# Optimization experiments

Hardware: AMD Instinct MI355X
Metric: run time of the kernel (lower is better)

The kernel has to match this reference:

```python
import jax, jax.numpy as jnp
import numpy as np

BS, SEQ, FT_IN = 64, 576, 768
HID, HEADS, FT_OUT = 512, 4, 512
N = SEQ + 1  # pooled node + tokens
NUM_NODES = BS * N


def _build_edges():
    # star graph per sample: 0 <-> (1+j) both directions, then self loops, batched with offsets
    j = np.arange(SEQ)
    src = np.empty(2 * SEQ, np.int32); dst = np.empty(2 * SEQ, np.int32)
    src[0::2] = 0;      dst[0::2] = 1 + j
    src[1::2] = 1 + j;  dst[1::2] = 0
    loops = np.arange(N, dtype=np.int32)
    src = np.concatenate([src, loops]); dst = np.concatenate([dst, loops])
    offs = (np.arange(BS, dtype=np.int32) * N)[:, None]
    return (src[None, :] + offs).reshape(-1), (dst[None, :] + offs).reshape(-1)


def setup_inputs() -> dict:
    key = jax.random.key(0)
    ks = jax.random.split(key, 24)
    s = 0.02
    src, dst = _build_edges()
    return {
        "hidden_states": jax.random.normal(ks[0], (BS, SEQ, FT_IN), jnp.float32),
        "pooled_output": jax.random.normal(ks[1], (BS, HID), jnp.float32),
        # SeqLinear projector: 768 -> 512 -> 512
        "pw1": jax.random.normal(ks[2], (FT_IN, HID)) * s, "pb1": jnp.zeros((HID,)),
        "pw2": jax.random.normal(ks[3], (HID, HID)) * s, "pb2": jnp.zeros((HID,)),
        # GATv2 conv1: 512 -> 4 heads x 128
        "wl1": jax.random.normal(ks[4], (HID, HID)) * s, "bl1": jnp.zeros((HID,)),
        "wr1": jax.random.normal(ks[5], (HID, HID)) * s, "br1": jnp.zeros((HID,)),
        "att1": jax.random.normal(ks[6], (HEADS, HID // HEADS)) * s,
        "bias1": jnp.zeros((HID,)),
        # GATv2 conv2: 512 -> 1 head x 512
        "wl2": jax.random.normal(ks[7], (HID, HID)) * s, "bl2": jnp.zeros((HID,)),
        "wr2": jax.random.normal(ks[8], (HID, HID)) * s, "br2": jnp.zeros((HID,)),
        "att2": jax.random.normal(ks[9], (1, HID)) * s,
        "bias2": jnp.zeros((HID,)),
        # final lin: 512 -> 512
        "linw": jax.random.normal(ks[10], (HID, FT_OUT)) * s, "linb": jnp.zeros((FT_OUT,)),
        "src": jnp.asarray(src), "dst": jnp.asarray(dst),
    }


def _gatv2(x, src, dst, wl, bl, wr, br, att, bias, heads, cout, num_nodes):
    # PyG GATv2Conv (share_weights=False), eval mode (attn dropout off)
    xl = (x @ wl + bl).reshape(num_nodes, heads, cout)  # source transform (messages)
    xr = (x @ wr + br).reshape(num_nodes, heads, cout)  # target transform
    z = jax.nn.leaky_relu(xl[src] + xr[dst], negative_slope=0.2)  # [E,H,C]
    e = jnp.einsum('ehc,hc->eh', z, att)                          # [E,H]
    m = jax.ops.segment_max(e, dst, num_segments=num_nodes)
    p = jnp.exp(e - m[dst])
    s = jax.ops.segment_sum(p, dst, num_segments=num_nodes)
    alpha = p / (s[dst] + 1e-16)                                  # segment softmax over in-edges
    out = jax.ops.segment_sum(xl[src] * alpha[..., None], dst, num_segments=num_nodes)
    return out.reshape(num_nodes, heads * cout) + bias


def reference(hidden_states, pooled_output, pw1, pb1, pw2, pb2,
              wl1, bl1, wr1, br1, att1, bias1,
              wl2, bl2, wr2, br2, att2, bias2,
              linw, linb, src, dst):
    bs, seq, _ = hidden_states.shape
    n = seq + 1
    num_nodes = bs * n
    # ProjLayers / SeqLinear (eval: dropout identity); GELU between layers
    h = jax.nn.gelu(hidden_states @ pw1 + pb1)
    h = h @ pw2 + pb2                                    # [bs, seq, 512]
    x = jnp.concatenate([pooled_output[:, None, :], h], axis=1)  # [bs, n, 512]
    x = x.reshape(num_nodes, -1)
    # GNN: GATv2 -> GELU -> GATv2
    h1 = jax.nn.gelu(_gatv2(x, src, dst, wl1, bl1, wr1, br1, att1, bias1, HEADS, HID // HEADS, num_nodes))
    h2 = _gatv2(h1, src, dst, wl2, bl2, wr2, br2, att2, bias2, 1, HID, num_nodes)
    h2b = h2.reshape(bs, n, -1)
    graph_mean = h2b.mean(axis=1)                        # global_mean_pool (contiguous graphs)
    cls = h2b[:, 0, :]                                   # node 0 per graph; dropout off (eval)
    out = cls @ linw + linb + pooled_output
    return out, graph_mean
```

## Files before the change

kernel.cpp:

```cpp
#include <hip/hip_runtime.h>
#include <hip/hip_bf16.h>
#include <math.h>

constexpr int BSZ       = 64;
constexpr int SEQL      = 576;
constexpr int FTIN      = 768;
constexpr int HID       = 512;
constexpr int NNODE     = SEQL + 1;
constexpr int NUM_NODES = BSZ * NNODE;
constexpr int MROWS     = BSZ * SEQL;

using b8 = __attribute__((ext_vector_type(8))) __bf16;
using f4 = __attribute__((ext_vector_type(4))) float;
typedef unsigned short u16;

__device__ __forceinline__ float gelu_f(float x) {
    float x3 = x * x * x;
    return 0.5f * x * (1.0f + tanhf(0.7978845608028654f * (x + 0.044715f * x3)));
}
__device__ __forceinline__ float lrelu(float x) {
    return x > 0.0f ? x : 0.2f * x;
}
__device__ __forceinline__ u16 f2bf(float v) {
    __hip_bfloat16 b = __float2bfloat16(v);
    return __builtin_bit_cast(u16, b);
}
__device__ __forceinline__ float bf2f(u16 u) {
    return __bfloat162float(__builtin_bit_cast(__hip_bfloat16, u));
}
__device__ __forceinline__ void split_bf(float v, u16& h, u16& l) {
    h = f2bf(v);
    l = f2bf(v - bf2f(h));
}
__device__ __forceinline__ void gl16(const void* g, void* l) {
    __builtin_amdgcn_global_load_lds(
        (const __attribute__((address_space(1))) unsigned int*)g,
        (__attribute__((address_space(3))) unsigned int*)l, 16, 0, 0);
}
__device__ __forceinline__ f4 mfma16(b8 a, b8 b, f4 c) {
    return __builtin_amdgcn_mfma_f32_16x16x32_bf16(a, b, c, 0, 0, 0);
}

__global__ __launch_bounds__(256) void transpose_split_k(
    const float* __restrict__ W, u16* __restrict__ Th,
    u16* __restrict__ Tl, int K, int N)
{
    __shared__ float t[64][65];
    const int kb = blockIdx.x * 64, nb = blockIdx.y * 64;
    for (int i = threadIdx.x; i < 64 * 64; i += 256) {
        int r = i >> 6, c = i & 63;
        t[r][c] = W[(size_t)(kb + r) * N + nb + c];
    }
    __syncthreads();
    for (int i = threadIdx.x; i < 64 * 64; i += 256) {
        int r = i >> 6, c = i & 63;
        float v = t[c][r];
        u16 h, l; split_bf(v, h, l);
        Th[(size_t)(nb + r) * K + kb + c] = h;
        Tl[(size_t)(nb + r) * K + kb + c] = l;
    }
}

__global__ __launch_bounds__(256) void fuse_bias_k(
    const float* __restrict__ pb,
    const float* __restrict__ wA, const float* __restrict__ wB,
    const float* __restrict__ bA, const float* __restrict__ bB,
    float* __restrict__ out)
{
    const int n = blockIdx.x * 256 + threadIdx.x;
    const float* W = (n < 512) ? wA : wB;
    const int c = n & 511;
    float acc = 0.0f;
    if (pb) {
        for (int j = 0; j < 512; j++) acc = fmaf(pb[j], W[(size_t)j * 512 + c], acc);
    }
    out[n] = acc + ((n < 512) ? bA[c] : bB[c]);
}

__global__ __launch_bounds__(256) void node0_proj_k(
    const float* __restrict__ pooled,
    const float* __restrict__ wl, const float* __restrict__ wr,
    const float* __restrict__ bl, const float* __restrict__ br,
    float* __restrict__ XL, float* __restrict__ XR)
{
    const int b = blockIdx.x;
    const int n = blockIdx.y * 256 + threadIdx.x;
    __shared__ float p[HID];
    for (int k = threadIdx.x; k < HID; k += 256) p[k] = pooled[b * HID + k];
    __syncthreads();
    const float* W = (n < 512) ? wl : wr;
    const int c = n & 511;
    float acc = 0.0f;
    for (int k = 0; k < HID; k++) acc = fmaf(p[k], W[(size_t)k * 512 + c], acc);
    acc += (n < 512) ? bl[c] : br[c];
    const size_t row = (size_t)b * NNODE * HID;
    if (n < 512) XL[row + c] = acc; else XR[row + c] = acc;
}

template<int MODE, bool AF32>
__global__ __launch_bounds__(256, 4) void bgemm(
    const u16* __restrict__ Ah, const u16* __restrict__ Al,
    const float* __restrict__ Af,
    const u16* __restrict__ BTh, const u16* __restrict__ BTl,
    const float* __restrict__ bias,
    float* __restrict__ CfL, float* __restrict__ CfR,
    u16* __restrict__ Ch, u16* __restrict__ Cl,
    int M, int K, int nblk)
{
    __shared__ u16 lds[4][4096];

    const int nwg = gridDim.x;
    const int p = blockIdx.x;
    const int lb = (nwg % 8 == 0) ? (p % 8) * (nwg / 8) + p / 8 : p;
    const int row0 = (lb / nblk) * 128, col0 = (lb % nblk) * 128;

    const int tid  = threadIdx.x;
    const int wid  = tid >> 6, lane = tid & 63;
    const int wr   = wid >> 1, wc = wid & 1;
    const int lrow = lane & 15, lk = lane >> 4;
    const int nt   = K >> 5;

    f4 acc[4][4] = {};
    float4 areg[4];

    for (int t = 0; t < nt; t++) {
        const int k0 = t << 5;

#pragma unroll
        for (int i = 0; i < 2; i++) {
            const int r = wid * 2 + i;
            const int bcol = col0 + r * 16 + lrow;
            const size_t bgo = (size_t)bcol * K + k0 + lk * 8;
            gl16(BTh + bgo, &lds[2][r * 512]);
            gl16(BTl + bgo, &lds[3][r * 512]);
            if constexpr (!AF32) {
                int grow = row0 + r * 16 + lrow;
                if (grow >= M) grow = M - 1;
                const size_t ago = (size_t)grow * K + k0 + lk * 8;
                gl16(Ah + ago, &lds[0][r * 512]);
                gl16(Al + ago, &lds[1][r * 512]);
            }
        }
        if constexpr (AF32) {
#pragma unroll
            for (int q = 0; q < 4; q++) {
                const int ch = tid * 4 + q;
                const int r = ch >> 3, c4 = ch & 7;
                areg[q] = *(const float4*)(Af + (size_t)(row0 + r) * K + k0 + c4 * 4);
            }
#pragma unroll
            for (int q = 0; q < 4; q++) {
                const int ch = tid * 4 + q;
                const int r = ch >> 3, c4 = ch & 7;
                u16 h0, l0, h1, l1, h2, l2, h3, l3;
                split_bf(areg[q].x, h0, l0); split_bf(areg[q].y, h1, l1);
                split_bf(areg[q].z, h2, l2); split_bf(areg[q].w, h3, l3);
                const int off = (r >> 4) * 512 + ((c4 >> 1) * 16 + (r & 15)) * 8 + (c4 & 1) * 4;
                *(ushort4*)&lds[0][off] = make_ushort4(h0, h1, h2, h3);
                *(ushort4*)&lds[1][off] = make_ushort4(l0, l1, l2, l3);
            }
        }
        __syncthreads();

        b8 a_h[4], b_h[4], tmp[4];
#pragma unroll
        for (int m = 0; m < 4; m++) a_h[m] = *(const b8*)&lds[0][(wr * 4 + m) * 512 + lane * 8];
#pragma unroll
        for (int n = 0; n < 4; n++) b_h[n] = *(const b8*)&lds[2][(wc * 4 + n) * 512 + lane * 8];
#pragma unroll
        for (int m = 0; m < 4; m++)
#pragma unroll
            for (int n = 0; n < 4; n++)
                acc[m][n] = mfma16(a_h[m], b_h[n], acc[m][n]);
#pragma unroll
        for (int m = 0; m < 4; m++) tmp[m] = *(const b8*)&lds[1][(wr * 4 + m) * 512 + lane * 8];
#pragma unroll
        for (int m = 0; m < 4; m++)
#pragma unroll
            for (int n = 0; n < 4; n++)
                acc[m][n] = mfma16(tmp[m], b_h[n], acc[m][n]);
#pragma unroll
        for (int n = 0; n < 4; n++) tmp[n] = *(const b8*)&lds[3][(wc * 4 + n) * 512 + lane * 8];
#pragma unroll
        for (int m = 0; m < 4; m++)
#pragma unroll
            for (int n = 0; n < 4; n++)
                acc[m][n] = mfma16(a_h[m], tmp[n], acc[m][n]);

        __syncthreads();
    }

    const int gcolbase = col0 + wc * 64;
    float biasn[4];
    if constexpr (MODE != 3) {
#pragma unroll
        for (int n = 0; n < 4; n++) biasn[n] = bias[gcolbase + n * 16 + lrow];
    }

#pragma unroll
    for (int m = 0; m < 4; m++) {
#pragma unroll
        for (int r = 0; r < 4; r++) {
            const int grow = row0 + wr * 64 + m * 16 + lk * 4 + r;
            if (MODE != 5 || grow < M) {
#pragma unroll
                for (int n = 0; n < 4; n++) {
                    const int gcol = gcolbase + n * 16 + lrow;
                    float v = acc[m][n][r];
                    if constexpr (MODE == 1) {
                        v = gelu_f(v + biasn[n]);
                        u16 h, l; split_bf(v, h, l);
                        Ch[(size_t)grow * HID + gcol] = h;
                        Cl[(size_t)grow * HID + gcol] = l;
                    } else if constexpr (MODE == 3) {
                        u16 h, l; split_bf(v, h, l);
                        Ch[(size_t)gcol * 512 + grow] = h;
                        Cl[(size_t)gcol * 512 + grow] = l;
                    } else {
                        v += biasn[n];
                        const int orow = (MODE == 4) ? (grow + grow / SEQL + 1) : grow;
                        if (gcol < 512) CfL[(size_t)orow * HID + gcol] = v;
                        else            CfR[(size_t)orow * HID + gcol - 512] = v;
                    }
                }
            }
        }
    }
}

template<int HEADS, bool GELU, bool OSPLIT>
__global__ __launch_bounds__(256) void gat_edge_k(
    const float* __restrict__ xl, const float* __restrict__ xr,
    const float* __restrict__ att, const float* __restrict__ bias,
    float* __restrict__ outF, u16* __restrict__ outH, u16* __restrict__ outL)
{
    const int b = blockIdx.x / SEQL;
    const int j = blockIdx.x % SEQL;
    const size_t row0 = (size_t)(b * NNODE) * HID;
    const size_t rowj = (size_t)(b * NNODE + 1 + j) * HID;
    const int t = threadIdx.x;
    const int c = 2 * t;

    const float2 xl0  = *(const float2*)(xl + row0 + c);
    const float2 xljv = *(const float2*)(xl + rowj + c);
    const float2 xrjv = *(const float2*)(xr + rowj + c);
    const float2 attc = *(const float2*)(att + c);

    float e0 = attc.x * lrelu(xl0.x + xrjv.x) + attc.y * lrelu(xl0.y + xrjv.y);
    float e1 = attc.x * lrelu(xljv.x + xrjv.x) + attc.y * lrelu(xljv.y + xrjv.y);

#pragma unroll
    for (int off = 32; off; off >>= 1) {
        e0 += __shfl_down(e0, off, 64);
        e1 += __shfl_down(e1, off, 64);
    }
    __shared__ float s0[4], s1[4];
    const int w = t >> 6, lane = t & 63;
    if (lane == 0) { s0[w] = e0; s1[w] = e1; }
    __syncthreads();

    float E0, E1;
    if (HEADS == 4) { E0 = s0[w]; E1 = s1[w]; }
    else            { E0 = s0[0] + s0[1] + s0[2] + s0[3];
                      E1 = s1[0] + s1[1] + s1[2] + s1[3]; }

    const float m  = fmaxf(E0, E1);
    const float p0 = expf(E0 - m);
    const float p1 = expf(E1 - m);
    const float inv = 1.0f / (p0 + p1 + 1e-16f);
    const float a0 = p0 * inv, a1 = p1 * inv;

    float ox = a0 * xl0.x + a1 * xljv.x + bias[c + 0];
    float oy = a0 * xl0.y + a1 * xljv.y + bias[c + 1];
    if (GELU) { ox = gelu_f(ox); oy = gelu_f(oy); }
    if constexpr (OSPLIT) {
        u16 h0, l0, h1, l1;
        split_bf(ox, h0, l0); split_bf(oy, h1, l1);
        *(ushort2*)&outH[rowj + c] = make_ushort2(h0, h1);
        *(ushort2*)&outL[rowj + c] = make_ushort2(l0, l1);
    } else {
        *(float2*)(outF + rowj + c) = make_float2(ox, oy);
    }
}

template<int HEADS, bool GELU, bool OSPLIT>
__global__ __launch_bounds__(256) void gat_node0_k(
    const float* __restrict__ xl, const float* __restrict__ xr,
    const float* __restrict__ att, const float* __restrict__ bias,
    float* __restrict__ outF, u16* __restrict__ outH, u16* __restrict__ outL)
{
    constexpr int CH = HID / HEADS;
    const int b = blockIdx.x;
    const int h = blockIdx.y;
    const int t = threadIdx.x;
    const size_t base = (size_t)(b * NNODE) * HID;

    __shared__ float xr0s[CH];
    __shared__ float es[NNODE];
    __shared__ float red[256];

    const float* atth = att + h * CH;
    for (int c = t; c < CH; c += 256) xr0s[c] = xr[base + h * CH + c];
    __syncthreads();

    for (int s = t; s < NNODE; s += 256) {
        const float* xls = xl + base + (size_t)s * HID + h * CH;
        float e = 0.0f;
        for (int c = 0; c < CH; c += 4) {
            float4 v = *(const float4*)(xls + c);
            float4 a = *(const float4*)(atth + c);
            e = fmaf(a.x, lrelu(v.x + xr0s[c + 0]), e);
            e = fmaf(a.y, lrelu(v.y + xr0s[c + 1]), e);
            e = fmaf(a.z, lrelu(v.z + xr0s[c + 2]), e);
            e = fmaf(a.w, lrelu(v.w + xr0s[c + 3]), e);
        }
        es[s] = e;
    }
    __syncthreads();

    float m = -INFINITY;
    for (int s = t; s < NNODE; s += 256) m = fmaxf(m, es[s]);
    red[t] = m; __syncthreads();
    for (int off = 128; off; off >>= 1) {
        if (t < off) red[t] = fmaxf(red[t], red[t + off]);
        __syncthreads();
    }
    m = red[0];
    __syncthreads();

    float sum = 0.0f;
    for (int s = t; s < NNODE; s += 256) {
        float p = expf(es[s] - m);
        es[s] = p;
        sum += p;
    }
    red[t] = sum; __syncthreads();
    for (int off = 128; off; off >>= 1) {
        if (t < off) red[t] += red[t + off];
        __syncthreads();
    }
    const float invS = 1.0f / (red[0] + 1e-16f);

    for (int c = t; c < CH; c += 256) {
        float acc = 0.0f;
        for (int s = 0; s < NNODE; s++)
            acc = fmaf(es[s], xl[base + (size_t)s * HID + h * CH + c], acc);
        float o = acc * invS + bias[h * CH + c];
        if (GELU) o = gelu_f(o);
        if constexpr (OSPLIT) {
            u16 hh, ll; split_bf(o, hh, ll);
            outH[base + h * CH + c] = hh;
            outL[base + h * CH + c] = ll;
        } else {
            outF[base + h * CH + c] = o;
        }
    }
}

__global__ __launch_bounds__(256) void mean_k(const float* __restrict__ h2,
                                              float* __restrict__ out)
{
    const int b = blockIdx.x;
    const int c = blockIdx.y * 256 + threadIdx.x;
    const float* p = h2 + (size_t)(b * NNODE) * HID + c;
    float s = 0.0f;
    for (int i = 0; i < NNODE; i++) s += p[(size_t)i * HID];
    out[(size_t)BSZ * HID + b * HID + c] = s * (1.0f / NNODE);
}

__global__ __launch_bounds__(256) void head_k(
    const float* __restrict__ h2, const float* __restrict__ linw,
    const float* __restrict__ linb, const float* __restrict__ pooled,
    float* __restrict__ out)
{
    const int b = blockIdx.x;
    const int col = blockIdx.y * 256 + threadIdx.x;
    __shared__ float cls[HID];
    for (int k = threadIdx.x; k < HID; k += 256)
        cls[k] = h2[(size_t)(b * NNODE) * HID + k];
    __syncthreads();
    float acc = 0.0f;
    for (int k = 0; k < HID; k++)
        acc = fmaf(cls[k], linw[(size_t)k * HID + col], acc);
    out[b * HID + col] = acc + linb[col] + pooled[b * HID + col];
}

extern "C" void kernel_launch(void* const* d_in, const int* in_sizes, int n_in,
                              void* d_out, int out_size, void* d_ws, size_t ws_size,
                              hipStream_t stream)
{
    const float* hs     = (const float*)d_in[0];
    const float* pooled = (const float*)d_in[1];
    const float* pw1  = (const float*)d_in[2];  const float* pb1   = (const float*)d_in[3];
    const float* pw2  = (const float*)d_in[4];  const float* pb2   = (const float*)d_in[5];
    const float* wl1  = (const float*)d_in[6];  const float* bl1   = (const float*)d_in[7];
    const float* wr1  = (const float*)d_in[8];  const float* br1   = (const float*)d_in[9];
    const float* att1 = (const float*)d_in[10]; const float* bias1 = (const float*)d_in[11];
    const float* wl2  = (const float*)d_in[12]; const float* bl2   = (const float*)d_in[13];
    const float* wr2  = (const float*)d_in[14]; const float* br2   = (const float*)d_in[15];
    const float* att2 = (const float*)d_in[16]; const float* bias2 = (const float*)d_in[17];
    const float* linw = (const float*)d_in[18]; const float* linb  = (const float*)d_in[19];
    float* out = (float*)d_out;

    char* ws = (char*)d_ws;
    const size_t RSZ = 75637760;
    char* R0 = ws;
    char* R1 = ws + RSZ;
    char* R2 = ws + 2 * RSZ;
    u16*  Wr = (u16*)(ws + 3 * RSZ);

    u16* hH  = (u16*)R0;
    u16* hL  = hH + (size_t)MROWS * HID;
    u16* h1H = (u16*)R0;
    u16* h1L = h1H + (size_t)NUM_NODES * HID;
    float* h2 = (float*)R0;
    float* XL = (float*)R1;
    float* XR = (float*)R2;
    u16* prepBT_h = (u16*)R1;
    u16* prepBT_l = prepBT_h + 1024 * 512;
    u16* pw1T_h   = prepBT_l + 1024 * 512;
    u16* pw1T_l   = pw1T_h + 512 * FTIN;
    u16* W1Th = Wr;
    u16* W1Tl = W1Th + 1024 * 512;
    u16* BT2h = W1Tl + 1024 * 512;
    u16* BT2l = BT2h + 1024 * 512;
    float* fb1 = (float*)(BT2l + 1024 * 512);
    float* fb2 = fb1 + 1024;

    const dim3 blk(256);

    transpose_split_k<<<dim3(8, 8), blk, 0, stream>>>(wl1, prepBT_h, prepBT_l, HID, HID);
    transpose_split_k<<<dim3(8, 8), blk, 0, stream>>>(wr1, prepBT_h + 512 * 512, prepBT_l + 512 * 512, HID, HID);
    transpose_split_k<<<dim3(12, 8), blk, 0, stream>>>(pw1, pw1T_h, pw1T_l, FTIN, HID);
    transpose_split_k<<<dim3(8, 8), blk, 0, stream>>>(wl2, BT2h, BT2l, HID, HID);
    transpose_split_k<<<dim3(8, 8), blk, 0, stream>>>(wr2, BT2h + 512 * 512, BT2l + 512 * 512, HID, HID);
    bgemm<3, true><<<dim3(32), blk, 0, stream>>>(nullptr, nullptr, pw2, prepBT_h, prepBT_l,
                                                 nullptr, nullptr, nullptr, W1Th, W1Tl, 512, HID, 8);
    fuse_bias_k<<<dim3(4), blk, 0, stream>>>(pb2, wl1, wr1, bl1, br1, fb1);
    fuse_bias_k<<<dim3(4), blk, 0, stream>>>(nullptr, wl2, wr2, bl2, br2, fb2);

    bgemm<1, true><<<dim3(1152), blk, 0, stream>>>(nullptr, nullptr, hs, pw1T_h, pw1T_l,
                                                   pb1, nullptr, nullptr, hH, hL, MROWS, FTIN, 4);
    bgemm<4, false><<<dim3(2304), blk, 0, stream>>>(hH, hL, nullptr, W1Th, W1Tl,
                                                    fb1, XL, XR, nullptr, nullptr, MROWS, HID, 8);
    node0_proj_k<<<dim3(BSZ, 4), blk, 0, stream>>>(pooled, wl1, wr1, bl1, br1, XL, XR);
    gat_edge_k<4, true, true><<<dim3(MROWS), blk, 0, stream>>>(XL, XR, att1, bias1,
                                                               nullptr, h1H, h1L);
    gat_node0_k<4, true, true><<<dim3(BSZ, 4), blk, 0, stream>>>(XL, XR, att1, bias1,
                                                                 nullptr, h1H, h1L);
    bgemm<5, false><<<dim3(2312), blk, 0, stream>>>(h1H, h1L, nullptr, BT2h, BT2l,
                                                    fb2, XL, XR, nullptr, nullptr, NUM_NODES, HID, 8);
    gat_edge_k<1, false, false><<<dim3(MROWS), blk, 0, stream>>>(XL, XR, att2, bias2,
                                                                 h2, nullptr, nullptr);
    gat_node0_k<1, false, false><<<dim3(BSZ, 1), blk, 0, stream>>>(XL, XR, att2, bias2,
                                                                   h2, nullptr, nullptr);
    head_k<<<dim3(BSZ, 2), blk, 0, stream>>>(h2, linw, linb, pooled, out);
    mean_k<<<dim3(BSZ, 2), blk, 0, stream>>>(h2, out);
}
```

Before: 1.078 ms.

## Split node-0 GAT aggregation into parallel multi-kernel pipeline and widen mean pooling

Replaces the single-block-per-(batch,head) node-0 attention kernel with four kernels. The first computes edge scores with one wavefront per source node and shuffle reductions. The second does the softmax max and sum per head, and the last two do the weighted sum over 8 node splits and then reduce the partials with bias, GELU and the output split. The old kernel had only 64–256 blocks running serial loops over 577 nodes, which left most of the GPU idle. Mean pooling is also split across four node chunks per block and eight column blocks. The price is extra launches and scratch buffers for scores and partial sums.

Result: faster. 951.7 us (-11.7%).

```diff
diff --git a/kernel.cpp b/kernel.cpp
--- a/kernel.cpp
+++ b/kernel.cpp
@@ -283,77 +283,116 @@
     }
 }
 
-template<int HEADS, bool GELU, bool OSPLIT>
-__global__ __launch_bounds__(256) void gat_node0_k(
-    const float* __restrict__ xl, const float* __restrict__ xr,
-    const float* __restrict__ att, const float* __restrict__ bias,
-    float* __restrict__ outF, u16* __restrict__ outH, u16* __restrict__ outL)
-{
-    constexpr int CH = HID / HEADS;
-    const int b = blockIdx.x;
-    const int h = blockIdx.y;
-    const int t = threadIdx.x;
-    const size_t base = (size_t)(b * NNODE) * HID;
-
-    __shared__ float xr0s[CH];
-    __shared__ float es[NNODE];
+template<int HEADS>
+__global__ __launch_bounds__(256) void n0a_k(
+    const float* __restrict__ XL, const float* __restrict__ XR,
+    const float* __restrict__ att, float* __restrict__ es)
+{
+    const int gs = blockIdx.x * 4 + (threadIdx.x >> 6);
+    const int lane = threadIdx.x & 63;
+    const int b = gs / NNODE, s = gs % NNODE;
+    const float* xls = XL + (size_t)(b * NNODE + s) * HID;
+    const float* xr0 = XR + (size_t)(b * NNODE) * HID;
+    const int c = lane * 8;
+    float e = 0.0f;
+#pragma unroll
+    for (int q = 0; q < 8; q += 4) {
+        const float4 v = *(const float4*)(xls + c + q);
+        const float4 r = *(const float4*)(xr0 + c + q);
+        const float4 a = *(const float4*)(att + c + q);
+        e = fmaf(a.x, lrelu(v.x + r.x), e);
+        e = fmaf(a.y, lrelu(v.y + r.y), e);
+        e = fmaf(a.z, lrelu(v.z + r.z), e);
+        e = fmaf(a.w, lrelu(v.w + r.w), e);
+    }
+    e += __shfl_xor(e, 1, 64);
+    e += __shfl_xor(e, 2, 64);
+    e += __shfl_xor(e, 4, 64);
+    e += __shfl_xor(e, 8, 64);
+    if (HEADS == 1) {
+        e += __shfl_xor(e, 16, 64);
+        e += __shfl_xor(e, 32, 64);
+        if (lane == 0) es[((size_t)b * NNODE + s) * 4] = e;
+    } else {
+        if ((lane & 15) == 0) es[((size_t)b * NNODE + s) * 4 + (lane >> 4)] = e;
+    }
+}
+
+__global__ __launch_bounds__(256) void n0b_k(float* __restrict__ es,
+                                             float* __restrict__ invS)
+{
+    const int b = blockIdx.x, h = blockIdx.y, t = threadIdx.x;
     __shared__ float red[256];
-
-    const float* atth = att + h * CH;
-    for (int c = t; c < CH; c += 256) xr0s[c] = xr[base + h * CH + c];
-    __syncthreads();
-
-    for (int s = t; s < NNODE; s += 256) {
-        const float* xls = xl + base + (size_t)s * HID + h * CH;
-        float e = 0.0f;
-        for (int c = 0; c < CH; c += 4) {
-            float4 v = *(const float4*)(xls + c);
-            float4 a = *(const float4*)(atth + c);
-            e = fmaf(a.x, lrelu(v.x + xr0s[c + 0]), e);
-            e = fmaf(a.y, lrelu(v.y + xr0s[c + 1]), e);
-            e = fmaf(a.z, lrelu(v.z + xr0s[c + 2]), e);
-            e = fmaf(a.w, lrelu(v.w + xr0s[c + 3]), e);
-        }
-        es[s] = e;
-    }
-    __syncthreads();
-
+    float* e = es + (size_t)b * NNODE * 4 + h;
     float m = -INFINITY;
-    for (int s = t; s < NNODE; s += 256) m = fmaxf(m, es[s]);
+    for (int s = t; s < NNODE; s += 256) m = fmaxf(m, e[(size_t)s * 4]);
     red[t] = m; __syncthreads();
-    for (int off = 128; off; off >>= 1) {
-        if (t < off) red[t] = fmaxf(red[t], red[t + off]);
+    for (int o = 128; o; o >>= 1) {
+        if (t < o) red[t] = fmaxf(red[t], red[t + o]);
         __syncthreads();
     }
-    m = red[0];
-    __syncthreads();
-
+    m = red[0]; __syncthreads();
     float sum = 0.0f;
     for (int s = t; s < NNODE; s += 256) {
-        float p = expf(es[s] - m);
-        es[s] = p;
+        const float p = expf(e[(size_t)s * 4] - m);
+        e[(size_t)s * 4] = p;
         sum += p;
     }
     red[t] = sum; __syncthreads();
-    for (int off = 128; off; off >>= 1) {
-        if (t < off) red[t] += red[t + off];
+    for (int o = 128; o; o >>= 1) {
+        if (t < o) red[t] += red[t + o];
         __syncthreads();
     }
-    const float invS = 1.0f / (red[0] + 1e-16f);
-
-    for (int c = t; c < CH; c += 256) {
-        float acc = 0.0f;
-        for (int s = 0; s < NNODE; s++)
-            acc = fmaf(es[s], xl[base + (size_t)s * HID + h * CH + c], acc);
-        float o = acc * invS + bias[h * CH + c];
-        if (GELU) o = gelu_f(o);
-        if constexpr (OSPLIT) {
-            u16 hh, ll; split_bf(o, hh, ll);
-            outH[base + h * CH + c] = hh;
-            outL[base + h * CH + c] = ll;
-        } else {
-            outF[base + h * CH + c] = o;
-        }
+    if (t == 0) invS[b * 4 + h] = 1.0f / (red[0] + 1e-16f);
+}
+
+template<int HEADS>
+__global__ __launch_bounds__(256) void n0c_k(
+    const float* __restrict__ XL, const float* __restrict__ es,
+    float* __restrict__ parts)
+{
+    const int b = blockIdx.x, split = blockIdx.y, t = threadIdx.x;
+    const int c = t * 2;
+    const int hh = (HEADS == 4) ? (c >> 7) : 0;
+    const int s0 = split * 73;
+    const int s1 = (s0 + 73 < NNODE) ? s0 + 73 : NNODE;
+    float ax = 0.0f, ay = 0.0f;
+    for (int s = s0; s < s1; s++) {
+        const float p = es[((size_t)b * NNODE + s) * 4 + hh];
+        const float2 v = *(const float2*)(XL + ((size_t)b * NNODE + s) * HID + c);
+        ax = fmaf(p, v.x, ax);
+        ay = fmaf(p, v.y, ay);
+    }
+    *(float2*)(parts + ((size_t)(b * 8 + split)) * HID + c) = make_float2(ax, ay);
+}
+
+template<int HEADS, bool GELU, bool OSPLIT>
+__global__ __launch_bounds__(256) void n0d_k(
+    const float* __restrict__ parts, const float* __restrict__ invS,
+    const float* __restrict__ bias,
+    float* __restrict__ outF, u16* __restrict__ outH, u16* __restrict__ outL)
+{
+    const int b = blockIdx.x, t = threadIdx.x;
+    const int c = t * 2;
+    const int hh = (HEADS == 4) ? (c >> 7) : 0;
+    float ax = 0.0f, ay = 0.0f;
+#pragma unroll
+    for (int sp = 0; sp < 8; sp++) {
+        const float2 v = *(const float2*)(parts + ((size_t)(b * 8 + sp)) * HID + c);
+        ax += v.x; ay += v.y;
+    }
+    const float is = invS[b * 4 + hh];
+    float ox = ax * is + bias[c];
+    float oy = ay * is + bias[c + 1];
+    if (GELU) { ox = gelu_f(ox); oy = gelu_f(oy); }
+    const size_t row = (size_t)b * NNODE * HID;
+    if constexpr (OSPLIT) {
+        u16 h0, l0, h1, l1;
+        split_bf(ox, h0, l0); split_bf(oy, h1, l1);
+        *(ushort2*)&outH[row + c] = make_ushort2(h0, h1);
+        *(ushort2*)&outL[row + c] = make_ushort2(l0, l1);
+    } else {
+        *(float2*)(outF + row + c) = make_float2(ox, oy);
     }
 }
 
@@ -361,11 +400,20 @@
                                               float* __restrict__ out)
 {
     const int b = blockIdx.x;
-    const int c = blockIdx.y * 256 + threadIdx.x;
-    const float* p = h2 + (size_t)(b * NNODE) * HID + c;
-    float s = 0.0f;
-    for (int i = 0; i < NNODE; i++) s += p[(size_t)i * HID];
-    out[(size_t)BSZ * HID + b * HID + c] = s * (1.0f / NNODE);
+    const int c = blockIdx.y * 64 + (threadIdx.x & 63);
+    const int chunk = threadIdx.x >> 6;
+    __shared__ float red[256];
+    const int s0 = chunk * 145;
+    const int s1 = (s0 + 145 < NNODE) ? s0 + 145 : NNODE;
+    const float* p = h2 + (size_t)b * NNODE * HID + c;
+    float acc = 0.0f;
+    for (int s = s0; s < s1; s++) acc += p[(size_t)s * HID];
+    red[threadIdx.x] = acc; __syncthreads();
+    if (threadIdx.x < 128) red[threadIdx.x] += red[threadIdx.x + 128];
+    __syncthreads();
+    if (threadIdx.x < 64)
+        out[(size_t)BSZ * HID + b * HID + blockIdx.y * 64 + threadIdx.x] =
+            (red[threadIdx.x] + red[threadIdx.x + 64]) * (1.0f / NNODE);
 }
 
 __global__ __launch_bounds__(256) void head_k(
@@ -426,6 +474,9 @@
     u16* BT2l = BT2h + 1024 * 512;
     float* fb1 = (float*)(BT2l + 1024 * 512);
     float* fb2 = fb1 + 1024;
+    float* esP  = fb2 + 1024;
+    float* invS = esP + (size_t)BSZ * NNODE * 4;
+    float* parts = invS + 256;
 
     const dim3 blk(256);
 
@@ -446,14 +497,20 @@
     node0_proj_k<<<dim3(BSZ, 4), blk, 0, stream>>>(pooled, wl1, wr1, bl1, br1, XL, XR);
     gat_edge_k<4, true, true><<<dim3(MROWS), blk, 0, stream>>>(XL, XR, att1, bias1,
                                                                nullptr, h1H, h1L);
-    gat_node0_k<4, true, true><<<dim3(BSZ, 4), blk, 0, stream>>>(XL, XR, att1, bias1,
-                                                                 nullptr, h1H, h1L);
+    n0a_k<4><<<dim3(NUM_NODES / 4), blk, 0, stream>>>(XL, XR, att1, esP);
+    n0b_k<<<dim3(BSZ, 4), blk, 0, stream>>>(esP, invS);
+    n0c_k<4><<<dim3(BSZ, 8), blk, 0, stream>>>(XL, esP, parts);
+    n0d_k<4, true, true><<<dim3(BSZ), blk, 0, stream>>>(parts, invS, bias1,
+                                                        nullptr, h1H, h1L);
     bgemm<5, false><<<dim3(2312), blk, 0, stream>>>(h1H, h1L, nullptr, BT2h, BT2l,
                                                     fb2, XL, XR, nullptr, nullptr, NUM_NODES, HID, 8);
     gat_edge_k<1, false, false><<<dim3(MROWS), blk, 0, stream>>>(XL, XR, att2, bias2,
                                                                  h2, nullptr, nullptr);
-    gat_node0_k<1, false, false><<<dim3(BSZ, 1), blk, 0, stream>>>(XL, XR, att2, bias2,
-                                                                   h2, nullptr, nullptr);
+    n0a_k<1><<<dim3(NUM_NODES / 4), blk, 0, stream>>>(XL, XR, att2, esP);
+    n0b_k<<<dim3(BSZ, 1), blk, 0, stream>>>(esP, invS);
+    n0c_k<1><<<dim3(BSZ, 8), blk, 0, stream>>>(XL, esP, parts);
+    n0d_k<1, false, false><<<dim3(BSZ), blk, 0, stream>>>(parts, invS, bias2,
+                                                          h2, nullptr, nullptr);
     head_k<<<dim3(BSZ, 2), blk, 0, stream>>>(h2, linw, linb, pooled, out);
-    mean_k<<<dim3(BSZ, 2), blk, 0, stream>>>(h2, out);
-}
+    mean_k<<<dim3(BSZ, 8), blk, 0, stream>>>(h2, out);
+}
```
